# Kernel tuning notes

Hardware: AMD Instinct MI355X
Metric: run time of the kernel (lower is better)

The kernel has to match this reference:

```python
import jax, jax.numpy as jnp
import numpy as np

H = 128      # config.hidden_dim
NH = 4       # config.attention_heads
NL = 2       # transformer encoder layers per encoder
FF = 2 * H   # dim_feedforward
B, R, T = 512, 50, 20
RDIM, TDIM = 7, 6
EPS = 1e-5


def setup_inputs():
    key = jax.random.key(0)
    ks = jax.random.split(key, 20)
    n = lambda k, shape, s=0.05: (jax.random.normal(k, shape) * s).astype(jnp.float32)
    z = lambda shape: jnp.zeros(shape, jnp.float32)
    o = lambda shape: jnp.ones(shape, jnp.float32)
    return {
        'robot_states': n(ks[0], (B, R, RDIM), 1.0),
        'task_states': n(ks[1], (B, T, TDIM), 1.0),
        'robot_proj_w': n(ks[2], (H, RDIM)), 'robot_proj_b': z((H,)),
        'task_proj_w': n(ks[3], (H, TDIM)), 'task_proj_b': z((H,)),
        # [encoder (0=robot,1=task), layer, ...]
        'enc_qkv_w': n(ks[4], (2, NL, 3 * H, H)), 'enc_qkv_b': z((2, NL, 3 * H)),
        'enc_out_w': n(ks[5], (2, NL, H, H)), 'enc_out_b': z((2, NL, H)),
        'enc_ff1_w': n(ks[6], (2, NL, FF, H)), 'enc_ff1_b': z((2, NL, FF)),
        'enc_ff2_w': n(ks[7], (2, NL, H, FF)), 'enc_ff2_b': z((2, NL, H)),
        'enc_ln1_g': o((2, NL, H)), 'enc_ln1_b': z((2, NL, H)),
        'enc_ln2_g': o((2, NL, H)), 'enc_ln2_b': z((2, NL, H)),
        'alloc_w1': n(ks[8], (H, 2 * H)), 'alloc_b1': z((H,)),
        'alloc_w2': n(ks[9], (1, H)), 'alloc_b2': z((1,)),
        'num_robots': R, 'num_tasks': T,
    }


def _ln(x, g, b):
    m = x.mean(-1, keepdims=True)
    v = ((x - m) ** 2).mean(-1, keepdims=True)
    return (x - m) / jnp.sqrt(v + EPS) * g + b


def _mha(x, qkv_w, qkv_b, out_w, out_b):
    Bx, S, Hd = x.shape
    dh = Hd // NH
    qkv = x @ qkv_w.T + qkv_b                      # [B,S,3H]
    q, k, v = jnp.split(qkv, 3, axis=-1)
    sp = lambda t: t.reshape(Bx, S, NH, dh).transpose(0, 2, 1, 3)  # [B,h,S,dh]
    q, k, v = sp(q), sp(k), sp(v)
    att = jax.nn.softmax(jnp.einsum('bhqd,bhkd->bhqk', q, k) * (1.0 / np.sqrt(dh)), axis=-1)
    o = jnp.einsum('bhqk,bhkd->bhqd', att, v).transpose(0, 2, 1, 3).reshape(Bx, S, Hd)
    return o @ out_w.T + out_b


def _encoder(x, e, qkv_w, qkv_b, out_w, out_b, ff1_w, ff1_b, ff2_w, ff2_b, ln1_g, ln1_b, ln2_g, ln2_b):
    # post-norm TransformerEncoderLayer (relu activation, eval mode -> no dropout)
    for l in range(NL):
        a = _mha(x, qkv_w[e, l], qkv_b[e, l], out_w[e, l], out_b[e, l])
        x = _ln(x + a, ln1_g[e, l], ln1_b[e, l])
        h = jax.nn.relu(x @ ff1_w[e, l].T + ff1_b[e, l]) @ ff2_w[e, l].T + ff2_b[e, l]
        x = _ln(x + h, ln2_g[e, l], ln2_b[e, l])
    return x


def reference(robot_states, task_states, robot_proj_w, robot_proj_b, task_proj_w, task_proj_b,
              enc_qkv_w, enc_qkv_b, enc_out_w, enc_out_b, enc_ff1_w, enc_ff1_b, enc_ff2_w, enc_ff2_b,
              enc_ln1_g, enc_ln1_b, enc_ln2_g, enc_ln2_b,
              enc_params_dummy=None, alloc_w1=None, alloc_b1=None, alloc_w2=None, alloc_b2=None,
              num_robots=R, num_tasks=T):
    raise NotImplementedError


def reference(robot_states, task_states, robot_proj_w, robot_proj_b, task_proj_w, task_proj_b,
              enc_qkv_w, enc_qkv_b, enc_out_w, enc_out_b, enc_ff1_w, enc_ff1_b, enc_ff2_w, enc_ff2_b,
              enc_ln1_g, enc_ln1_b, enc_ln2_g, enc_ln2_b,
              alloc_w1, alloc_b1, alloc_w2, alloc_b2, num_robots, num_tasks):
    ep = (enc_qkv_w, enc_qkv_b, enc_out_w, enc_out_b, enc_ff1_w, enc_ff1_b,
          enc_ff2_w, enc_ff2_b, enc_ln1_g, enc_ln1_b, enc_ln2_g, enc_ln2_b)
    r = robot_states[:, :num_robots] @ robot_proj_w.T + robot_proj_b   # [B,R,H]
    t = task_states[:, :num_tasks] @ task_proj_w.T + task_proj_b      # [B,T,H]
    rf = _encoder(r, 0, *ep)
    tf = _encoder(t, 1, *ep)
    # fused pairwise concat+MLP: concat([task, robot]) @ w1.T == task@w1[:, :H].T + robot@w1[:, H:].T
    a = tf @ alloc_w1[:, :H].T                                          # [B,T,H]
    b = rf @ alloc_w1[:, H:].T                                          # [B,R,H]
    h = jax.nn.relu(a[:, :, None, :] + b[:, None, :, :] + alloc_b1)     # [B,T,R,H]
    scores = (h @ alloc_w2.T + alloc_b2)[..., 0]                        # [B,T,R]
    return jax.nn.softmax(scores, axis=-1)
```

## Files before the change

kernel.cpp:

```cpp
#include <hip/hip_runtime.h>
#include <hip/hip_bf16.h>


#define HD    128
#define NHEAD 4
#define DHEAD 32
#define NLAY  2
#define FFD   256
#define BB    512
#define RR    50
#define TT    20
#define RD    7
#define TD    6
#define EPSV  1e-5f

#define NRROW (BB*RR)
#define NTROW (BB*TT)

using bf16 = __hip_bfloat16;
typedef __attribute__((ext_vector_type(8))) short short8;
typedef __attribute__((ext_vector_type(4))) float f32x4;

__device__ __forceinline__ float b2f(bf16 x) { return __bfloat162float(x); }

__device__ __forceinline__ float ldg1(const void* p, size_t i, int f) {
    return f ? ((const float*)p)[i] : b2f(((const bf16*)p)[i]);
}

__device__ __forceinline__ unsigned pack2(float a, float b) {
    union { bf16 h; unsigned short u; } x, y;
    x.h = __float2bfloat16(a); y.h = __float2bfloat16(b);
    return (unsigned)x.u | ((unsigned)y.u << 16);
}

__device__ __forceinline__ void st_bf16(unsigned char* p, float v) {
    bf16 h = __float2bfloat16(v);
    *reinterpret_cast<short*>(p) = *reinterpret_cast<const short*>(&h);
}

__global__ void probe_kernel(const unsigned* __restrict__ g, int* __restrict__ flag) {
    if (threadIdx.x == 0) flag[0] = (g[0] == 0x3F800000u) ? 1 : 0;
}

#define NWQ (2*NLAY*3*HD*HD)
#define NWO (2*NLAY*HD*HD)
#define NW1 (2*NLAY*FFD*HD)
#define NW2 (2*NLAY*HD*FFD)
#define NWMAIN (NWQ+NWO+NW1+NW2)
#define NWSPL (HD*HD)

__global__ void convall_kernel(const void* __restrict__ qkv_w, const void* __restrict__ out_w,
                               const void* __restrict__ ff1_w, const void* __restrict__ ff2_w,
                               const void* __restrict__ alloc_w1, bf16* __restrict__ wbf,
                               const int* __restrict__ flag) {
    const int f = flag[0];
    const int i = blockIdx.x * 256 + threadIdx.x;
    if (i < NWQ) {
        wbf[i] = __float2bfloat16(ldg1(qkv_w, i, f));
    } else if (i < NWQ + NWO) {
        wbf[i] = __float2bfloat16(ldg1(out_w, i - NWQ, f));
    } else if (i < NWQ + NWO + NW1) {
        wbf[i] = __float2bfloat16(ldg1(ff1_w, i - NWQ - NWO, f));
    } else if (i < NWMAIN) {
        wbf[i] = __float2bfloat16(ldg1(ff2_w, i - NWQ - NWO - NW1, f));
    } else if (i < NWMAIN + NWSPL) {
        const int idx = i - NWMAIN;
        const int j = idx >> 7, k = idx & 127;
        wbf[NWMAIN + idx]         = __float2bfloat16(ldg1(alloc_w1, (size_t)j * 256 + k, f));
        wbf[NWMAIN + NWSPL + idx] = __float2bfloat16(ldg1(alloc_w1, (size_t)j * 256 + 128 + k, f));
    }
}

template<int S, int SPAD, int KD>
__device__ __forceinline__ void enc_body(
    unsigned char* sm, int bid, float* __restrict__ xg,
    const void* __restrict__ states, const void* __restrict__ pw, const void* __restrict__ pbias,
    const bf16* __restrict__ wqB, const void* __restrict__ bqv,
    const bf16* __restrict__ woB, const void* __restrict__ bov,
    const bf16* __restrict__ w1B, const void* __restrict__ b1v,
    const bf16* __restrict__ w2B, const void* __restrict__ b2v,
    const void* __restrict__ g1v, const void* __restrict__ be1v,
    const void* __restrict__ g2v, const void* __restrict__ be2v,
    int enc, int f)
{
    constexpr int NMT = SPAD / 16;
    constexpr int CTN = SPAD / 16;
    constexpr int KT2 = SPAD / 32;
    constexpr int PM  = (SPAD * 2 >= 128) ? 7 : 3;
    constexpr int OFF_XB = 0;
    constexpr int OFF_B  = SPAD * 256;
    constexpr int OFF_C  = OFF_B + SPAD * 512;

    const int tid  = threadIdx.x;
    const int wid  = tid >> 6;
    const int lane = tid & 63;
    const int g    = lane >> 4;
    const int cl   = lane & 15;
    float* xrow = xg + (size_t)bid * S * HD;

    {
        float* ws = (float*)(sm + OFF_B);
        float* st = ws + HD * KD;
        float* pb = st + S * KD;
        for (int i = tid; i < HD * KD; i += 256) ws[i] = ldg1(pw, i, f);
        for (int i = tid; i < S * KD; i += 256)
            st[i] = ldg1(states, (size_t)bid * S * KD + i, f);
        if (tid < HD) pb[tid] = ldg1(pbias, tid, f);
        __syncthreads();
        for (int i = tid; i < SPAD * HD; i += 256) {
            const int r = i >> 7, c = i & 127;
            float val = 0.f;
            if (r < S) {
                val = pb[c];
#pragma unroll
                for (int k = 0; k < KD; ++k) val += st[r * KD + k] * ws[c * KD + k];
                xrow[r * HD + c] = val;
            }
            st_bf16(sm + OFF_XB + r * 256 + ((c * 2) ^ ((r & 7) << 4)), val);
        }
    }
    __syncthreads();

#pragma unroll 1
    for (int l = 0; l < NLAY; ++l) {
        const size_t li = (size_t)(enc * NLAY + l);
        const bf16* wq = wqB + li * 3 * HD * HD;

#pragma unroll
        for (int t2 = 0; t2 < 4; ++t2) {
            const int n = (wid * 4 + t2) * 16 + cl;
            const float bias = ldg1(bqv, li * 3 * HD + n, f);
            f32x4 acc[NMT];
#pragma unroll
            for (int mt = 0; mt < NMT; ++mt) acc[mt] = (f32x4){0.f, 0.f, 0.f, 0.f};
#pragma unroll
            for (int kt = 0; kt < 4; ++kt) {
                const short8 bw = *reinterpret_cast<const short8*>(wq + (size_t)n * HD + kt * 32 + g * 8);
#pragma unroll
                for (int mt = 0; mt < NMT; ++mt) {
                    const int ar = mt * 16 + cl;
                    const short8 a = *reinterpret_cast<const short8*>(
                        sm + OFF_XB + ar * 256 + ((kt * 64 + g * 16) ^ ((ar & 7) << 4)));
                    acc[mt] = __builtin_amdgcn_mfma_f32_16x16x32_bf16(a, bw, acc[mt], 0, 0, 0);
                }
            }
#pragma unroll
            for (int mt = 0; mt < NMT; ++mt)
#pragma unroll
                for (int j = 0; j < 4; ++j) {
                    const int row = mt * 16 + g * 4 + j;
                    st_bf16(sm + OFF_B + row * 512 + ((n * 2) ^ ((row & 7) << 4)), acc[mt][j] + bias);
                }
        }
#pragma unroll
        for (int t2 = 0; t2 < 2; ++t2) {
            const int n = (16 + wid * 2 + t2) * 16 + cl;
            const int d = n - 256;
            const float bias = ldg1(bqv, li * 3 * HD + n, f);
            f32x4 acc[NMT];
#pragma unroll
            for (int mt = 0; mt < NMT; ++mt) acc[mt] = (f32x4){0.f, 0.f, 0.f, 0.f};
#pragma unroll
            for (int kt = 0; kt < 4; ++kt) {
                const short8 bw = *reinterpret_cast<const short8*>(wq + (size_t)n * HD + kt * 32 + g * 8);
#pragma unroll
                for (int mt = 0; mt < NMT; ++mt) {
                    const int ar = mt * 16 + cl;
                    const short8 a = *reinterpret_cast<const short8*>(
                        sm + OFF_XB + ar * 256 + ((kt * 64 + g * 16) ^ ((ar & 7) << 4)));
                    acc[mt] = __builtin_amdgcn_mfma_f32_16x16x32_bf16(a, bw, acc[mt], 0, 0, 0);
                }
            }
#pragma unroll
            for (int mt = 0; mt < NMT; ++mt)
#pragma unroll
                for (int j = 0; j < 4; ++j) {
                    const int row = mt * 16 + g * 4 + j;
                    st_bf16(sm + OFF_C + d * (SPAD * 2) + ((row * 2) ^ ((d & PM) << 4)), acc[mt][j] + bias);
                }
        }
        __syncthreads();

        {
            const int h = wid;
            short8 aq[NMT], bk[CTN];
#pragma unroll
            for (int mt = 0; mt < NMT; ++mt) {
                const int row = mt * 16 + cl;
                aq[mt] = *reinterpret_cast<const short8*>(
                    sm + OFF_B + row * 512 + ((h * 64 + g * 16) ^ ((row & 7) << 4)));
            }
#pragma unroll
            for (int ct = 0; ct < CTN; ++ct) {
                const int kr = ct * 16 + cl;
                bk[ct] = *reinterpret_cast<const short8*>(
                    sm + OFF_B + kr * 512 + ((256 + h * 64 + g * 16) ^ ((kr & 7) << 4)));
            }
            __syncthreads();

            unsigned char* pb2 = sm + OFF_B + wid * (SPAD * SPAD * 2);
            const float scale = 0.17677669529663687f;
#pragma unroll
            for (int mt = 0; mt < NMT; ++mt) {
                f32x4 scr[CTN];
#pragma unroll
                for (int ct = 0; ct < CTN; ++ct)
                    scr[ct] = __builtin_amdgcn_mfma_f32_16x16x32_bf16(
                        aq[mt], bk[ct], (f32x4){0.f, 0.f, 0.f, 0.f}, 0, 0, 0);
#pragma unroll
                for (int j = 0; j < 4; ++j) {
                    float v[CTN];
                    float m = -1e30f;
#pragma unroll
                    for (int ct = 0; ct < CTN; ++ct) {
                        const float x = scr[ct][j] * scale;
                        v[ct] = (ct * 16 + cl < S) ? x : -1e30f;
                        m = fmaxf(m, v[ct]);
                    }
#pragma unroll
                    for (int off = 1; off < 16; off <<= 1) m = fmaxf(m, __shfl_xor(m, off));
                    float sum = 0.f;
#pragma unroll
                    for (int ct = 0; ct < CTN; ++ct) { v[ct] = __expf(v[ct] - m); sum += v[ct]; }
#pragma unroll
                    for (int off = 1; off < 16; off <<= 1) sum += __shfl_xor(sum, off);
                    const float inv = 1.f / sum;
                    const int row = mt * 16 + g * 4 + j;
#pragma unroll
                    for (int ct = 0; ct < CTN; ++ct) {
                        const int col = ct * 16 + cl;
                        st_bf16(pb2 + row * (SPAD * 2) + ((col * 2) ^ ((row & PM) << 4)), v[ct] * inv);
                    }
                }
            }

            f32x4 o[NMT][2];
#pragma unroll
            for (int mt = 0; mt < NMT; ++mt) {
                o[mt][0] = (f32x4){0.f, 0.f, 0.f, 0.f};
                o[mt][1] = (f32x4){0.f, 0.f, 0.f, 0.f};
            }
#pragma unroll
            for (int kt2 = 0; kt2 < KT2; ++kt2) {
#pragma unroll
                for (int dt = 0; dt < 2; ++dt) {
                    const int d = h * 32 + dt * 16 + cl;
                    const short8 bv = *reinterpret_cast<const short8*>(
                        sm + OFF_C + d * (SPAD * 2) + ((kt2 * 64 + g * 16) ^ ((d & PM) << 4)));
#pragma unroll
                    for (int mt = 0; mt < NMT; ++mt) {
                        const int row = mt * 16 + cl;
                        const short8 ap = *reinterpret_cast<const short8*>(
                            pb2 + row * (SPAD * 2) + ((kt2 * 64 + g * 16) ^ ((row & PM) << 4)));
                        o[mt][dt] = __builtin_amdgcn_mfma_f32_16x16x32_bf16(ap, bv, o[mt][dt], 0, 0, 0);
                    }
                }
            }
            __syncthreads();

#pragma unroll
            for (int mt = 0; mt < NMT; ++mt)
#pragma unroll
                for (int dt = 0; dt < 2; ++dt)
#pragma unroll
                    for (int j = 0; j < 4; ++j) {
                        const int row = mt * 16 + g * 4 + j;
                        const int col = h * 32 + dt * 16 + cl;
                        st_bf16(sm + OFF_C + row * 256 + ((col * 2) ^ ((row & 7) << 4)), o[mt][dt][j]);
                    }
        }
        __syncthreads();

        float tv[2][NMT][4];
#pragma unroll
        for (int ntl = 0; ntl < 2; ++ntl) {
            const int n = (wid * 2 + ntl) * 16 + cl;
#pragma unroll
            for (int mt = 0; mt < NMT; ++mt)
#pragma unroll
                for (int j = 0; j < 4; ++j) {
                    const int row = mt * 16 + g * 4 + j;
                    tv[ntl][mt][j] = (row < S) ? xrow[row * HD + n] : 0.f;
                }
        }
        {
            const bf16* wo = woB + li * HD * HD;
#pragma unroll
            for (int ntl = 0; ntl < 2; ++ntl) {
                const int n = (wid * 2 + ntl) * 16 + cl;
                const float bias = ldg1(bov, li * HD + n, f);
                f32x4 acc[NMT];
#pragma unroll
                for (int mt = 0; mt < NMT; ++mt) acc[mt] = (f32x4){0.f, 0.f, 0.f, 0.f};
#pragma unroll
                for (int kt = 0; kt < 4; ++kt) {
                    const short8 bw = *reinterpret_cast<const short8*>(wo + (size_t)n * HD + kt * 32 + g * 8);
#pragma unroll
                    for (int mt = 0; mt < NMT; ++mt) {
                        const int ar = mt * 16 + cl;
                        const short8 a = *reinterpret_cast<const short8*>(
                            sm + OFF_C + ar * 256 + ((kt * 64 + g * 16) ^ ((ar & 7) << 4)));
                        acc[mt] = __builtin_amdgcn_mfma_f32_16x16x32_bf16(a, bw, acc[mt], 0, 0, 0);
                    }
                }
#pragma unroll
                for (int mt = 0; mt < NMT; ++mt)
#pragma unroll
                    for (int j = 0; j < 4; ++j)
                        tv[ntl][mt][j] += acc[mt][j] + bias;
            }
        }
        {
            float* p1 = (float*)(sm + OFF_B);
            float* p2 = p1 + 4 * SPAD;
#pragma unroll
            for (int mt = 0; mt < NMT; ++mt)
#pragma unroll
                for (int j = 0; j < 4; ++j) {
                    float s1 = tv[0][mt][j] + tv[1][mt][j];
                    float s2 = tv[0][mt][j] * tv[0][mt][j] + tv[1][mt][j] * tv[1][mt][j];
#pragma unroll
                    for (int off = 1; off < 16; off <<= 1) {
                        s1 += __shfl_xor(s1, off);
                        s2 += __shfl_xor(s2, off);
                    }
                    if (cl == 0) {
                        const int row = mt * 16 + g * 4 + j;
                        p1[wid * SPAD + row] = s1;
                        p2[wid * SPAD + row] = s2;
                    }
                }
            __syncthreads();
#pragma unroll
            for (int ntl = 0; ntl < 2; ++ntl) {
                const int n = (wid * 2 + ntl) * 16 + cl;
                const float gam = ldg1(g1v, li * HD + n, f);
                const float bet = ldg1(be1v, li * HD + n, f);
#pragma unroll
                for (int mt = 0; mt < NMT; ++mt)
#pragma unroll
                    for (int j = 0; j < 4; ++j) {
                        const int row = mt * 16 + g * 4 + j;
                        const float mean = (p1[row] + p1[SPAD + row] + p1[2 * SPAD + row] + p1[3 * SPAD + row]) * (1.f / HD);
                        const float var  = (p2[row] + p2[SPAD + row] + p2[2 * SPAD + row] + p2[3 * SPAD + row]) * (1.f / HD) - mean * mean;
                        const float y = (tv[ntl][mt][j] - mean) * rsqrtf(var + EPSV) * gam + bet;
                        tv[ntl][mt][j] = y;
                        if (row < S)
                            st_bf16(sm + OFF_XB + row * 256 + ((n * 2) ^ ((row & 7) << 4)), y);
                    }
            }
        }
        __syncthreads();

        {
            const bf16* w1 = w1B + li * FFD * HD;
#pragma unroll
            for (int t2 = 0; t2 < 4; ++t2) {
                const int n = (wid * 4 + t2) * 16 + cl;
                const float bias = ldg1(b1v, li * FFD + n, f);
                f32x4 acc[NMT];
#pragma unroll
                for (int mt = 0; mt < NMT; ++mt) acc[mt] = (f32x4){0.f, 0.f, 0.f, 0.f};
#pragma unroll
                for (int kt = 0; kt < 4; ++kt) {
                    const short8 bw = *reinterpret_cast<const short8*>(w1 + (size_t)n * HD + kt * 32 + g * 8);
#pragma unroll
                    for (int mt = 0; mt < NMT; ++mt) {
                        const int ar = mt * 16 + cl;
                        const short8 a = *reinterpret_cast<const short8*>(
                            sm + OFF_XB + ar * 256 + ((kt * 64 + g * 16) ^ ((ar & 7) << 4)));
                        acc[mt] = __builtin_amdgcn_mfma_f32_16x16x32_bf16(a, bw, acc[mt], 0, 0, 0);
                    }
                }
#pragma unroll
                for (int mt = 0; mt < NMT; ++mt)
#pragma unroll
                    for (int j = 0; j < 4; ++j) {
                        const int row = mt * 16 + g * 4 + j;
                        st_bf16(sm + OFF_B + row * 512 + ((n * 2) ^ ((row & 7) << 4)),
                                fmaxf(acc[mt][j] + bias, 0.f));
                    }
            }
        }
        __syncthreads();

        {
            const bf16* w2 = w2B + li * HD * FFD;
#pragma unroll
            for (int ntl = 0; ntl < 2; ++ntl) {
                const int n = (wid * 2 + ntl) * 16 + cl;
                const float bias = ldg1(b2v, li * HD + n, f);
                f32x4 acc[NMT];
#pragma unroll
                for (int mt = 0; mt < NMT; ++mt) acc[mt] = (f32x4){0.f, 0.f, 0.f, 0.f};
#pragma unroll
                for (int kt = 0; kt < 8; ++kt) {
                    const short8 bw = *reinterpret_cast<const short8*>(w2 + (size_t)n * FFD + kt * 32 + g * 8);
#pragma unroll
                    for (int mt = 0; mt < NMT; ++mt) {
                        const int ar = mt * 16 + cl;
                        const short8 a = *reinterpret_cast<const short8*>(
                            sm + OFF_B + ar * 512 + ((kt * 64 + g * 16) ^ ((ar & 7) << 4)));
                        acc[mt] = __builtin_amdgcn_mfma_f32_16x16x32_bf16(a, bw, acc[mt], 0, 0, 0);
                    }
                }
#pragma unroll
                for (int mt = 0; mt < NMT; ++mt)
#pragma unroll
                    for (int j = 0; j < 4; ++j)
                        tv[ntl][mt][j] = acc[mt][j] + bias + tv[ntl][mt][j];
            }
            float* q1 = (float*)(sm + OFF_C);
            float* q2 = q1 + 4 * SPAD;
#pragma unroll
            for (int mt = 0; mt < NMT; ++mt)
#pragma unroll
                for (int j = 0; j < 4; ++j) {
                    float s1 = tv[0][mt][j] + tv[1][mt][j];
                    float s2 = tv[0][mt][j] * tv[0][mt][j] + tv[1][mt][j] * tv[1][mt][j];
#pragma unroll
                    for (int off = 1; off < 16; off <<= 1) {
                        s1 += __shfl_xor(s1, off);
                        s2 += __shfl_xor(s2, off);
                    }
                    if (cl == 0) {
                        const int row = mt * 16 + g * 4 + j;
                        q1[wid * SPAD + row] = s1;
                        q2[wid * SPAD + row] = s2;
                    }
                }
            __syncthreads();
#pragma unroll
            for (int ntl = 0; ntl < 2; ++ntl) {
                const int n = (wid * 2 + ntl) * 16 + cl;
                const float gam = ldg1(g2v, li * HD + n, f);
                const float bet = ldg1(be2v, li * HD + n, f);
#pragma unroll
                for (int mt = 0; mt < NMT; ++mt)
#pragma unroll
                    for (int j = 0; j < 4; ++j) {
                        const int row = mt * 16 + g * 4 + j;
                        const float mean = (q1[row] + q1[SPAD + row] + q1[2 * SPAD + row] + q1[3 * SPAD + row]) * (1.f / HD);
                        const float var  = (q2[row] + q2[SPAD + row] + q2[2 * SPAD + row] + q2[3 * SPAD + row]) * (1.f / HD) - mean * mean;
                        const float y = (tv[ntl][mt][j] - mean) * rsqrtf(var + EPSV) * gam + bet;
                        if (row < S) {
                            st_bf16(sm + OFF_XB + row * 256 + ((n * 2) ^ ((row & 7) << 4)), y);
                            xrow[row * HD + n] = y;
                        }
                    }
            }
        }
        __syncthreads();
    }
}

__global__ __launch_bounds__(256, 1) void enc17_kernel(
    float* __restrict__ xr, float* __restrict__ xt,
    const void* __restrict__ rstates, const void* __restrict__ rpw, const void* __restrict__ rpb,
    const void* __restrict__ tstates, const void* __restrict__ tpw, const void* __restrict__ tpb,
    const bf16* __restrict__ wqB, const void* __restrict__ bqv,
    const bf16* __restrict__ woB, const void* __restrict__ bov,
    const bf16* __restrict__ w1B, const void* __restrict__ b1v,
    const bf16* __restrict__ w2B, const void* __restrict__ b2v,
    const void* __restrict__ g1v, const void* __restrict__ be1v,
    const void* __restrict__ g2v, const void* __restrict__ be2v,
    const int* __restrict__ flag)
{
    __shared__ __attribute__((aligned(16))) unsigned char sm[64 * 1024];
    const int f = flag[0];
    if (blockIdx.x < BB)
        enc_body<RR, 64, RD>(sm, blockIdx.x, xr, rstates, rpw, rpb,
                             wqB, bqv, woB, bov, w1B, b1v, w2B, b2v,
                             g1v, be1v, g2v, be2v, 0, f);
    else
        enc_body<TT, 32, TD>(sm, blockIdx.x - BB, xt, tstates, tpw, tpb,
                             wqB, bqv, woB, bov, w1B, b1v, w2B, b2v,
                             g1v, be1v, g2v, be2v, 1, f);
}

__global__ __launch_bounds__(256) void scoref_kernel(
    const float* __restrict__ xt, const float* __restrict__ xr,
    const bf16* __restrict__ wa, const bf16* __restrict__ wb,
    const void* __restrict__ b1, const void* __restrict__ w2,
    const void* __restrict__ b2p, void* __restrict__ out,
    const int* __restrict__ flag)
{
    const int f = flag[0];
    const int b = blockIdx.x;
    __shared__ __attribute__((aligned(16))) short xts[32 * 128];
    __shared__ __attribute__((aligned(16))) short xrs[64 * 128];
    __shared__ float sa[TT][129];
    __shared__ float sb[RR][129];
    __shared__ float w2s[HD];
    float* scb = (float*)xts;

    const int tid = threadIdx.x;
    const int wid = tid >> 6, lane = tid & 63;
    const int g = lane >> 4, cl = lane & 15;

    for (int i = tid; i < 32 * 128 / 4; i += 256) {
        const int idx = i * 4;
        const int r = idx >> 7, c = idx & 127;
        float4 v = {0.f, 0.f, 0.f, 0.f};
        if (r < TT) v = *reinterpret_cast<const float4*>(xt + ((size_t)b * TT + r) * HD + c);
        uint2 pk; pk.x = pack2(v.x, v.y); pk.y = pack2(v.z, v.w);
        *reinterpret_cast<uint2*>((unsigned char*)xts + r * 256 + ((c * 2) ^ ((r & 7) << 4))) = pk;
    }
    for (int i = tid; i < 64 * 128 / 4; i += 256) {
        const int idx = i * 4;
        const int r = idx >> 7, c = idx & 127;
        float4 v = {0.f, 0.f, 0.f, 0.f};
        if (r < RR) v = *reinterpret_cast<const float4*>(xr + ((size_t)b * RR + r) * HD + c);
        uint2 pk; pk.x = pack2(v.x, v.y); pk.y = pack2(v.z, v.w);
        *reinterpret_cast<uint2*>((unsigned char*)xrs + r * 256 + ((c * 2) ^ ((r & 7) << 4))) = pk;
    }
    if (tid < HD) w2s[tid] = ldg1(w2, tid, f);
    __syncthreads();

#pragma unroll
    for (int q = 0; q < 4; ++q) {
        const int job = wid * 4 + q;
        const int rt = job >> 3, nt = job & 7;
        const int n = nt * 16 + cl;
        f32x4 acc = (f32x4){0.f, 0.f, 0.f, 0.f};
#pragma unroll
        for (int kt = 0; kt < 4; ++kt) {
            const short8 bw = *reinterpret_cast<const short8*>(wa + (size_t)n * HD + kt * 32 + g * 8);
            const int ar = rt * 16 + cl;
            const short8 a = *reinterpret_cast<const short8*>(
                (unsigned char*)xts + ar * 256 + ((kt * 64 + g * 16) ^ ((ar & 7) << 4)));
            acc = __builtin_amdgcn_mfma_f32_16x16x32_bf16(a, bw, acc, 0, 0, 0);
        }
        const float bias = ldg1(b1, n, f);
#pragma unroll
        for (int j = 0; j < 4; ++j) {
            const int row = rt * 16 + g * 4 + j;
            if (row < TT) sa[row][n] = acc[j] + bias;
        }
    }
#pragma unroll
    for (int q = 0; q < 8; ++q) {
        const int job = wid * 8 + q;
        const int rt = job >> 3, nt = job & 7;
        const int n = nt * 16 + cl;
        f32x4 acc = (f32x4){0.f, 0.f, 0.f, 0.f};
#pragma unroll
        for (int kt = 0; kt < 4; ++kt) {
            const short8 bw = *reinterpret_cast<const short8*>(wb + (size_t)n * HD + kt * 32 + g * 8);
            const int ar = rt * 16 + cl;
            const short8 a = *reinterpret_cast<const short8*>(
                (unsigned char*)xrs + ar * 256 + ((kt * 64 + g * 16) ^ ((ar & 7) << 4)));
            acc = __builtin_amdgcn_mfma_f32_16x16x32_bf16(a, bw, acc, 0, 0, 0);
        }
#pragma unroll
        for (int j = 0; j < 4; ++j) {
            const int row = rt * 16 + g * 4 + j;
            if (row < RR) sb[row][n] = acc[j];
        }
    }
    __syncthreads();

    const float bias2 = ldg1(b2p, 0, f);
    for (int p = tid; p < TT * RR; p += 256) {
        const int t = p / RR, r = p % RR;
        float acc = 0.f;
#pragma unroll 16
        for (int k = 0; k < HD; ++k)
            acc += fmaxf(sa[t][k] + sb[r][k], 0.f) * w2s[k];
        scb[t * 52 + r] = acc + bias2;
    }
    __syncthreads();

    for (int t = wid; t < TT; t += 4) {
        const float val = (lane < RR) ? scb[t * 52 + lane] : -1e30f;
        float m = val;
#pragma unroll
        for (int off = 32; off > 0; off >>= 1) m = fmaxf(m, __shfl_xor(m, off));
        const float e = (lane < RR) ? __expf(val - m) : 0.f;
        float s = e;
#pragma unroll
        for (int off = 32; off > 0; off >>= 1) s += __shfl_xor(s, off);
        if (lane < RR) {
            const float r = e / s;
            const size_t idx = (size_t)(b * TT + t) * RR + lane;
            if (f) ((float*)out)[idx] = r;
            else   ((bf16*)out)[idx] = __float2bfloat16(r);
        }
    }
}

extern "C" void kernel_launch(void* const* d_in, const int* in_sizes, int n_in,
                              void* d_out, int out_size, void* d_ws, size_t ws_size,
                              hipStream_t stream) {
    const void* robot_states = d_in[0];
    const void* task_states  = d_in[1];
    const void* rproj_w = d_in[2];
    const void* rproj_b = d_in[3];
    const void* tproj_w = d_in[4];
    const void* tproj_b = d_in[5];
    const void* qkv_w = d_in[6];
    const void* qkv_b = d_in[7];
    const void* out_w = d_in[8];
    const void* out_b = d_in[9];
    const void* ff1_w = d_in[10];
    const void* ff1_b = d_in[11];
    const void* ff2_w = d_in[12];
    const void* ff2_b = d_in[13];
    const void* ln1_g = d_in[14];
    const void* ln1_b = d_in[15];
    const void* ln2_g = d_in[16];
    const void* ln2_b = d_in[17];
    const void* alloc_w1 = d_in[18];
    const void* alloc_b1 = d_in[19];
    const void* alloc_w2 = d_in[20];
    const void* alloc_b2 = d_in[21];
    (void)in_sizes; (void)n_in; (void)out_size; (void)ws_size;

    float* xr    = (float*)d_ws;
    float* xt    = xr + (size_t)NRROW * HD;
    float* scratch = xt + (size_t)NTROW * HD;
    int*   flag  = (int*)scratch;
    bf16*  wbf   = (bf16*)(scratch + 4);

    bf16* wq_bf = wbf;
    bf16* wo_bf = wq_bf + NWQ;
    bf16* w1_bf = wo_bf + NWO;
    bf16* w2_bf = w1_bf + NW1;
    bf16* wa_bf = w2_bf + NW2;
    bf16* wb_bf = wa_bf + NWSPL;

    probe_kernel<<<1, 64, 0, stream>>>((const unsigned*)ln1_g, flag);

    convall_kernel<<<(NWMAIN + NWSPL + 255) / 256, 256, 0, stream>>>(
        qkv_w, out_w, ff1_w, ff2_w, alloc_w1, wbf, flag);

    enc17_kernel<<<2 * BB, 256, 0, stream>>>(
        xr, xt,
        robot_states, rproj_w, rproj_b,
        task_states, tproj_w, tproj_b,
        wq_bf, qkv_b, wo_bf, out_b, w1_bf, ff1_b, w2_bf, ff2_b,
        ln1_g, ln1_b, ln2_g, ln2_b, flag);

    scoref_kernel<<<BB, 256, 0, stream>>>(
        xt, xr, wa_bf, wb_bf, alloc_b1, alloc_w2, alloc_b2, d_out, flag);
}
```

Baseline: 254.4 us.

## Double encoder block to 512 threads, splitting work across eight waves

The fused encoder kernel now launches 512 threads (8 waves) per block instead of 256. Each wave owns half as many output column tiles in the QKV, out-proj, FF1 and FF2 GEMMs, and attention uses two waves per head, each taking half the query row tiles. LayerNorm partial sums are reduced across eight waves instead of four. The aim is more latency hiding and fewer per-wave registers, paid for with more barrier participants and less reuse of each A-operand load per wave.

```diff
diff --git a/kernel.cpp b/kernel.cpp
--- a/kernel.cpp
+++ b/kernel.cpp
@@ -83,10 +83,11 @@
     const void* __restrict__ g2v, const void* __restrict__ be2v,
     int enc, int f)
 {
-    constexpr int NMT = SPAD / 16;
-    constexpr int CTN = SPAD / 16;
-    constexpr int KT2 = SPAD / 32;
-    constexpr int PM  = (SPAD * 2 >= 128) ? 7 : 3;
+    constexpr int NMT  = SPAD / 16;
+    constexpr int NMT2 = NMT / 2;
+    constexpr int CTN  = SPAD / 16;
+    constexpr int KT2  = SPAD / 32;
+    constexpr int PM   = (SPAD * 2 >= 128) ? 7 : 3;
     constexpr int OFF_XB = 0;
     constexpr int OFF_B  = SPAD * 256;
     constexpr int OFF_C  = OFF_B + SPAD * 512;
@@ -102,12 +103,12 @@
         float* ws = (float*)(sm + OFF_B);
         float* st = ws + HD * KD;
         float* pb = st + S * KD;
-        for (int i = tid; i < HD * KD; i += 256) ws[i] = ldg1(pw, i, f);
-        for (int i = tid; i < S * KD; i += 256)
+        for (int i = tid; i < HD * KD; i += 512) ws[i] = ldg1(pw, i, f);
+        for (int i = tid; i < S * KD; i += 512)
             st[i] = ldg1(states, (size_t)bid * S * KD + i, f);
         if (tid < HD) pb[tid] = ldg1(pbias, tid, f);
         __syncthreads();
-        for (int i = tid; i < SPAD * HD; i += 256) {
+        for (int i = tid; i < SPAD * HD; i += 512) {
             const int r = i >> 7, c = i & 127;
             float val = 0.f;
             if (r < S) {
@@ -127,8 +128,8 @@
         const bf16* wq = wqB + li * 3 * HD * HD;
 
 #pragma unroll
-        for (int t2 = 0; t2 < 4; ++t2) {
-            const int n = (wid * 4 + t2) * 16 + cl;
+        for (int t2 = 0; t2 < 2; ++t2) {
+            const int n = (wid * 2 + t2) * 16 + cl;
             const float bias = ldg1(bqv, li * 3 * HD + n, f);
             f32x4 acc[NMT];
 #pragma unroll
@@ -152,10 +153,9 @@
                     st_bf16(sm + OFF_B + row * 512 + ((n * 2) ^ ((row & 7) << 4)), acc[mt][j] + bias);
                 }
         }
-#pragma unroll
-        for (int t2 = 0; t2 < 2; ++t2) {
-            const int n = (16 + wid * 2 + t2) * 16 + cl;
-            const int d = n - 256;
+        {
+            const int n = (16 + wid) * 16 + cl;
+            const int d = wid * 16 + cl;
             const float bias = ldg1(bqv, li * 3 * HD + n, f);
             f32x4 acc[NMT];
 #pragma unroll
@@ -182,12 +182,13 @@
         __syncthreads();
 
         {
-            const int h = wid;
-            short8 aq[NMT], bk[CTN];
-#pragma unroll
-            for (int mt = 0; mt < NMT; ++mt) {
-                const int row = mt * 16 + cl;
-                aq[mt] = *reinterpret_cast<const short8*>(
+            const int h   = wid >> 1;
+            const int sub = wid & 1;
+            short8 aq[NMT2], bk[CTN];
+#pragma unroll
+            for (int m = 0; m < NMT2; ++m) {
+                const int row = (sub * NMT2 + m) * 16 + cl;
+                aq[m] = *reinterpret_cast<const short8*>(
                     sm + OFF_B + row * 512 + ((h * 64 + g * 16) ^ ((row & 7) << 4)));
             }
 #pragma unroll
@@ -198,34 +199,34 @@
             }
             __syncthreads();
 
-            unsigned char* pb2 = sm + OFF_B + wid * (SPAD * SPAD * 2);
+            unsigned char* pb2 = sm + OFF_B + h * (SPAD * SPAD * 2);
             const float scale = 0.17677669529663687f;
 #pragma unroll
-            for (int mt = 0; mt < NMT; ++mt) {
+            for (int m = 0; m < NMT2; ++m) {
                 f32x4 scr[CTN];
 #pragma unroll
                 for (int ct = 0; ct < CTN; ++ct)
                     scr[ct] = __builtin_amdgcn_mfma_f32_16x16x32_bf16(
-                        aq[mt], bk[ct], (f32x4){0.f, 0.f, 0.f, 0.f}, 0, 0, 0);
+                        aq[m], bk[ct], (f32x4){0.f, 0.f, 0.f, 0.f}, 0, 0, 0);
 #pragma unroll
                 for (int j = 0; j < 4; ++j) {
                     float v[CTN];
-                    float m = -1e30f;
+                    float mx = -1e30f;
 #pragma unroll
                     for (int ct = 0; ct < CTN; ++ct) {
                         const float x = scr[ct][j] * scale;
                         v[ct] = (ct * 16 + cl < S) ? x : -1e30f;
-                        m = fmaxf(m, v[ct]);
-                    }
-#pragma unroll
-                    for (int off = 1; off < 16; off <<= 1) m = fmaxf(m, __shfl_xor(m, off));
+                        mx = fmaxf(mx, v[ct]);
+                    }
+#pragma unroll
+                    for (int off = 1; off < 16; off <<= 1) mx = fmaxf(mx, __shfl_xor(mx, off));
                     float sum = 0.f;
 #pragma unroll
-                    for (int ct = 0; ct < CTN; ++ct) { v[ct] = __expf(v[ct] - m); sum += v[ct]; }
+                    for (int ct = 0; ct < CTN; ++ct) { v[ct] = __expf(v[ct] - mx); sum += v[ct]; }
 #pragma unroll
                     for (int off = 1; off < 16; off <<= 1) sum += __shfl_xor(sum, off);
                     const float inv = 1.f / sum;
-                    const int row = mt * 16 + g * 4 + j;
+                    const int row = (sub * NMT2 + m) * 16 + g * 4 + j;
 #pragma unroll
                     for (int ct = 0; ct < CTN; ++ct) {
                         const int col = ct * 16 + cl;
@@ -234,11 +235,11 @@
                 }
             }
 
-            f32x4 o[NMT][2];
-#pragma unroll
-            for (int mt = 0; mt < NMT; ++mt) {
-                o[mt][0] = (f32x4){0.f, 0.f, 0.f, 0.f};
-                o[mt][1] = (f32x4){0.f, 0.f, 0.f, 0.f};
+            f32x4 o[NMT2][2];
+#pragma unroll
+            for (int m = 0; m < NMT2; ++m) {
+                o[m][0] = (f32x4){0.f, 0.f, 0.f, 0.f};
+                o[m][1] = (f32x4){0.f, 0.f, 0.f, 0.f};
             }
 #pragma unroll
             for (int kt2 = 0; kt2 < KT2; ++kt2) {
@@ -248,77 +249,70 @@
                     const short8 bv = *reinterpret_cast<const short8*>(
                         sm + OFF_C + d * (SPAD * 2) + ((kt2 * 64 + g * 16) ^ ((d & PM) << 4)));
 #pragma unroll
-                    for (int mt = 0; mt < NMT; ++mt) {
-                        const int row = mt * 16 + cl;
+                    for (int m = 0; m < NMT2; ++m) {
+                        const int row = (sub * NMT2 + m) * 16 + cl;
                         const short8 ap = *reinterpret_cast<const short8*>(
                             pb2 + row * (SPAD * 2) + ((kt2 * 64 + g * 16) ^ ((row & PM) << 4)));
-                        o[mt][dt] = __builtin_amdgcn_mfma_f32_16x16x32_bf16(ap, bv, o[mt][dt], 0, 0, 0);
+                        o[m][dt] = __builtin_amdgcn_mfma_f32_16x16x32_bf16(ap, bv, o[m][dt], 0, 0, 0);
                     }
                 }
             }
             __syncthreads();
 
 #pragma unroll
-            for (int mt = 0; mt < NMT; ++mt)
+            for (int m = 0; m < NMT2; ++m)
 #pragma unroll
                 for (int dt = 0; dt < 2; ++dt)
 #pragma unroll
                     for (int j = 0; j < 4; ++j) {
-                        const int row = mt * 16 + g * 4 + j;
+                        const int row = (sub * NMT2 + m) * 16 + g * 4 + j;
                         const int col = h * 32 + dt * 16 + cl;
-                        st_bf16(sm + OFF_C + row * 256 + ((col * 2) ^ ((row & 7) << 4)), o[mt][dt][j]);
+                        st_bf16(sm + OFF_C + row * 256 + ((col * 2) ^ ((row & 7) << 4)), o[m][dt][j]);
                     }
         }
         __syncthreads();
 
-        float tv[2][NMT][4];
-#pragma unroll
-        for (int ntl = 0; ntl < 2; ++ntl) {
-            const int n = (wid * 2 + ntl) * 16 + cl;
-#pragma unroll
-            for (int mt = 0; mt < NMT; ++mt)
-#pragma unroll
-                for (int j = 0; j < 4; ++j) {
-                    const int row = mt * 16 + g * 4 + j;
-                    tv[ntl][mt][j] = (row < S) ? xrow[row * HD + n] : 0.f;
-                }
-        }
+        float tv[NMT][4];
+        const int nn = wid * 16 + cl;
+#pragma unroll
+        for (int mt = 0; mt < NMT; ++mt)
+#pragma unroll
+            for (int j = 0; j < 4; ++j) {
+                const int row = mt * 16 + g * 4 + j;
+                tv[mt][j] = (row < S) ? xrow[row * HD + nn] : 0.f;
+            }
         {
             const bf16* wo = woB + li * HD * HD;
-#pragma unroll
-            for (int ntl = 0; ntl < 2; ++ntl) {
-                const int n = (wid * 2 + ntl) * 16 + cl;
-                const float bias = ldg1(bov, li * HD + n, f);
-                f32x4 acc[NMT];
-#pragma unroll
-                for (int mt = 0; mt < NMT; ++mt) acc[mt] = (f32x4){0.f, 0.f, 0.f, 0.f};
-#pragma unroll
-                for (int kt = 0; kt < 4; ++kt) {
-                    const short8 bw = *reinterpret_cast<const short8*>(wo + (size_t)n * HD + kt * 32 + g * 8);
-#pragma unroll
-                    for (int mt = 0; mt < NMT; ++mt) {
-                        const int ar = mt * 16 + cl;
-                        const short8 a = *reinterpret_cast<const short8*>(
-                            sm + OFF_C + ar * 256 + ((kt * 64 + g * 16) ^ ((ar & 7) << 4)));
-                        acc[mt] = __builtin_amdgcn_mfma_f32_16x16x32_bf16(a, bw, acc[mt], 0, 0, 0);
-                    }
-                }
-#pragma unroll
-                for (int mt = 0; mt < NMT; ++mt)
-#pragma unroll
-                    for (int j = 0; j < 4; ++j)
-                        tv[ntl][mt][j] += acc[mt][j] + bias;
-            }
+            const float bias = ldg1(bov, li * HD + nn, f);
+            f32x4 acc[NMT];
+#pragma unroll
+            for (int mt = 0; mt < NMT; ++mt) acc[mt] = (f32x4){0.f, 0.f, 0.f, 0.f};
+#pragma unroll
+            for (int kt = 0; kt < 4; ++kt) {
+                const short8 bw = *reinterpret_cast<const short8*>(wo + (size_t)nn * HD + kt * 32 + g * 8);
+#pragma unroll
+                for (int mt = 0; mt < NMT; ++mt) {
+                    const int ar = mt * 16 + cl;
+                    const short8 a = *reinterpret_cast<const short8*>(
+                        sm + OFF_C + ar * 256 + ((kt * 64 + g * 16) ^ ((ar & 7) << 4)));
+                    acc[mt] = __builtin_amdgcn_mfma_f32_16x16x32_bf16(a, bw, acc[mt], 0, 0, 0);
+                }
+            }
+#pragma unroll
+            for (int mt = 0; mt < NMT; ++mt)
+#pragma unroll
+                for (int j = 0; j < 4; ++j)
+                    tv[mt][j] += acc[mt][j] + bias;
         }
         {
             float* p1 = (float*)(sm + OFF_B);
-            float* p2 = p1 + 4 * SPAD;
+            float* p2 = p1 + 8 * SPAD;
 #pragma unroll
             for (int mt = 0; mt < NMT; ++mt)
 #pragma unroll
                 for (int j = 0; j < 4; ++j) {
-                    float s1 = tv[0][mt][j] + tv[1][mt][j];
-                    float s2 = tv[0][mt][j] * tv[0][mt][j] + tv[1][mt][j] * tv[1][mt][j];
+                    float s1 = tv[mt][j];
+                    float s2 = tv[mt][j] * tv[mt][j];
 #pragma unroll
                     for (int off = 1; off < 16; off <<= 1) {
                         s1 += __shfl_xor(s1, off);
@@ -331,32 +325,34 @@
                     }
                 }
             __syncthreads();
-#pragma unroll
-            for (int ntl = 0; ntl < 2; ++ntl) {
-                const int n = (wid * 2 + ntl) * 16 + cl;
-                const float gam = ldg1(g1v, li * HD + n, f);
-                const float bet = ldg1(be1v, li * HD + n, f);
-#pragma unroll
-                for (int mt = 0; mt < NMT; ++mt)
-#pragma unroll
-                    for (int j = 0; j < 4; ++j) {
-                        const int row = mt * 16 + g * 4 + j;
-                        const float mean = (p1[row] + p1[SPAD + row] + p1[2 * SPAD + row] + p1[3 * SPAD + row]) * (1.f / HD);
-                        const float var  = (p2[row] + p2[SPAD + row] + p2[2 * SPAD + row] + p2[3 * SPAD + row]) * (1.f / HD) - mean * mean;
-                        const float y = (tv[ntl][mt][j] - mean) * rsqrtf(var + EPSV) * gam + bet;
-                        tv[ntl][mt][j] = y;
-                        if (row < S)
-                            st_bf16(sm + OFF_XB + row * 256 + ((n * 2) ^ ((row & 7) << 4)), y);
-                    }
-            }
+            const float gam = ldg1(g1v, li * HD + nn, f);
+            const float bet = ldg1(be1v, li * HD + nn, f);
+#pragma unroll
+            for (int mt = 0; mt < NMT; ++mt)
+#pragma unroll
+                for (int j = 0; j < 4; ++j) {
+                    const int row = mt * 16 + g * 4 + j;
+                    float sum = 0.f, sumsq = 0.f;
+#pragma unroll
+                    for (int w = 0; w < 8; ++w) {
+                        sum   += p1[w * SPAD + row];
+                        sumsq += p2[w * SPAD + row];
+                    }
+                    const float mean = sum * (1.f / HD);
+                    const float var  = sumsq * (1.f / HD) - mean * mean;
+                    const float y = (tv[mt][j] - mean) * rsqrtf(var + EPSV) * gam + bet;
+                    tv[mt][j] = y;
+                    if (row < S)
+                        st_bf16(sm + OFF_XB + row * 256 + ((nn * 2) ^ ((row & 7) << 4)), y);
+                }
         }
         __syncthreads();
 
         {
             const bf16* w1 = w1B + li * FFD * HD;
 #pragma unroll
-            for (int t2 = 0; t2 < 4; ++t2) {
-                const int n = (wid * 4 + t2) * 16 + cl;
+            for (int t2 = 0; t2 < 2; ++t2) {
+                const int n = (wid * 2 + t2) * 16 + cl;
                 const float bias = ldg1(b1v, li * FFD + n, f);
                 f32x4 acc[NMT];
 #pragma unroll
@@ -386,38 +382,35 @@
 
         {
             const bf16* w2 = w2B + li * HD * FFD;
-#pragma unroll
-            for (int ntl = 0; ntl < 2; ++ntl) {
-                const int n = (wid * 2 + ntl) * 16 + cl;
-                const float bias = ldg1(b2v, li * HD + n, f);
-                f32x4 acc[NMT];
-#pragma unroll
-                for (int mt = 0; mt < NMT; ++mt) acc[mt] = (f32x4){0.f, 0.f, 0.f, 0.f};
-#pragma unroll
-                for (int kt = 0; kt < 8; ++kt) {
-                    const short8 bw = *reinterpret_cast<const short8*>(w2 + (size_t)n * FFD + kt * 32 + g * 8);
-#pragma unroll
-                    for (int mt = 0; mt < NMT; ++mt) {
-                        const int ar = mt * 16 + cl;
-                        const short8 a = *reinterpret_cast<const short8*>(
-                            sm + OFF_B + ar * 512 + ((kt * 64 + g * 16) ^ ((ar & 7) << 4)));
-                        acc[mt] = __builtin_amdgcn_mfma_f32_16x16x32_bf16(a, bw, acc[mt], 0, 0, 0);
-                    }
-                }
-#pragma unroll
-                for (int mt = 0; mt < NMT; ++mt)
-#pragma unroll
-                    for (int j = 0; j < 4; ++j)
-                        tv[ntl][mt][j] = acc[mt][j] + bias + tv[ntl][mt][j];
-            }
+            const float bias = ldg1(b2v, li * HD + nn, f);
+            f32x4 acc[NMT];
+#pragma unroll
+            for (int mt = 0; mt < NMT; ++mt) acc[mt] = (f32x4){0.f, 0.f, 0.f, 0.f};
+#pragma unroll
+            for (int kt = 0; kt < 8; ++kt) {
+                const short8 bw = *reinterpret_cast<const short8*>(w2 + (size_t)nn * FFD + kt * 32 + g * 8);
+#pragma unroll
+                for (int mt = 0; mt < NMT; ++mt) {
+                    const int ar = mt * 16 + cl;
+                    const short8 a = *reinterpret_cast<const short8*>(
+                        sm + OFF_B + ar * 512 + ((kt * 64 + g * 16) ^ ((ar & 7) << 4)));
+                    acc[mt] = __builtin_amdgcn_mfma_f32_16x16x32_bf16(a, bw, acc[mt], 0, 0, 0);
+                }
+            }
+#pragma unroll
+            for (int mt = 0; mt < NMT; ++mt)
+#pragma unroll
+                for (int j = 0; j < 4; ++j)
+                    tv[mt][j] = acc[mt][j] + bias + tv[mt][j];
+
             float* q1 = (float*)(sm + OFF_C);
-            float* q2 = q1 + 4 * SPAD;
+            float* q2 = q1 + 8 * SPAD;
 #pragma unroll
             for (int mt = 0; mt < NMT; ++mt)
 #pragma unroll
                 for (int j = 0; j < 4; ++j) {
-                    float s1 = tv[0][mt][j] + tv[1][mt][j];
-                    float s2 = tv[0][mt][j] * tv[0][mt][j] + tv[1][mt][j] * tv[1][mt][j];
+                    float s1 = tv[mt][j];
+                    float s2 = tv[mt][j] * tv[mt][j];
 #pragma unroll
                     for (int off = 1; off < 16; off <<= 1) {
                         s1 += __shfl_xor(s1, off);
@@ -430,31 +423,33 @@
                     }
                 }
             __syncthreads();
-#pragma unroll
-            for (int ntl = 0; ntl < 2; ++ntl) {
-                const int n = (wid * 2 + ntl) * 16 + cl;
-                const float gam = ldg1(g2v, li * HD + n, f);
-                const float bet = ldg1(be2v, li * HD + n, f);
-#pragma unroll
-                for (int mt = 0; mt < NMT; ++mt)
-#pragma unroll
-                    for (int j = 0; j < 4; ++j) {
-                        const int row = mt * 16 + g * 4 + j;
-                        const float mean = (q1[row] + q1[SPAD + row] + q1[2 * SPAD + row] + q1[3 * SPAD + row]) * (1.f / HD);
-                        const float var  = (q2[row] + q2[SPAD + row] + q2[2 * SPAD + row] + q2[3 * SPAD + row]) * (1.f / HD) - mean * mean;
-                        const float y = (tv[ntl][mt][j] - mean) * rsqrtf(var + EPSV) * gam + bet;
-                        if (row < S) {
-                            st_bf16(sm + OFF_XB + row * 256 + ((n * 2) ^ ((row & 7) << 4)), y);
-                            xrow[row * HD + n] = y;
-                        }
-                    }
-            }
+            const float gam = ldg1(g2v, li * HD + nn, f);
+            const float bet = ldg1(be2v, li * HD + nn, f);
+#pragma unroll
+            for (int mt = 0; mt < NMT; ++mt)
+#pragma unroll
+                for (int j = 0; j < 4; ++j) {
+                    const int row = mt * 16 + g * 4 + j;
+                    float sum = 0.f, sumsq = 0.f;
+#pragma unroll
+                    for (int w = 0; w < 8; ++w) {
+                        sum   += q1[w * SPAD + row];
+                        sumsq += q2[w * SPAD + row];
+                    }
+                    const float mean = sum * (1.f / HD);
+                    const float var  = sumsq * (1.f / HD) - mean * mean;
+                    const float y = (tv[mt][j] - mean) * rsqrtf(var + EPSV) * gam + bet;
+                    if (row < S) {
+                        st_bf16(sm + OFF_XB + row * 256 + ((nn * 2) ^ ((row & 7) << 4)), y);
+                        xrow[row * HD + nn] = y;
+                    }
+                }
         }
         __syncthreads();
     }
 }
 
-__global__ __launch_bounds__(256, 1) void enc17_kernel(
+__global__ __launch_bounds__(512) void enc18_kernel(
     float* __restrict__ xr, float* __restrict__ xt,
     const void* __restrict__ rstates, const void* __restrict__ rpw, const void* __restrict__ rpb,
     const void* __restrict__ tstates, const void* __restrict__ tpw, const void* __restrict__ tpb,
@@ -634,7 +629,7 @@
     convall_kernel<<<(NWMAIN + NWSPL + 255) / 256, 256, 0, stream>>>(
         qkv_w, out_w, ff1_w, ff2_w, alloc_w1, wbf, flag);
 
-    enc17_kernel<<<2 * BB, 256, 0, stream>>>(
+    enc18_kernel<<<2 * BB, 512, 0, stream>>>(
         xr, xt,
         robot_states, rproj_w, rproj_b,
         task_states, tproj_w, tproj_b,
```

Result: slower. 298.3 us (+17.3%).
